# Optimization experiments

Hardware: AMD Instinct MI355X
Metric: run time of the kernel (lower is better)

The kernel has to match this reference:

```python
import jax, jax.numpy as jnp
import numpy as np

BATCH = 1024
DIM = 1024      # input_size == hidden_size (required by h0 = z.repeat(...))
BAR = 32
EPS = 1e-5


def setup_inputs() -> dict:
    key = jax.random.key(0)
    ks = jax.random.split(key, 13)
    s_in = 1.0 / np.sqrt(DIM)
    return {
        "z": jax.random.normal(ks[0], (BATCH, DIM), dtype=jnp.float32),
        "bn_gamma": jnp.ones((DIM,), jnp.float32),
        "bn_beta": jnp.zeros((DIM,), jnp.float32),
        # PyTorch LSTM params, gate order (i, f, g, o), shape (4H, in)
        "W_ih0": jax.random.uniform(ks[1], (4 * DIM, DIM), jnp.float32, -s_in, s_in),
        "W_hh0": jax.random.uniform(ks[2], (4 * DIM, DIM), jnp.float32, -s_in, s_in),
        "b_ih0": jax.random.uniform(ks[3], (4 * DIM,), jnp.float32, -s_in, s_in),
        "b_hh0": jax.random.uniform(ks[4], (4 * DIM,), jnp.float32, -s_in, s_in),
        "W_ih1": jax.random.uniform(ks[5], (4 * DIM, DIM), jnp.float32, -s_in, s_in),
        "W_hh1": jax.random.uniform(ks[6], (4 * DIM, DIM), jnp.float32, -s_in, s_in),
        "b_ih1": jax.random.uniform(ks[7], (4 * DIM,), jnp.float32, -s_in, s_in),
        "b_hh1": jax.random.uniform(ks[8], (4 * DIM,), jnp.float32, -s_in, s_in),
        "W_lin": jax.random.uniform(ks[9], (DIM, DIM), jnp.float32, -s_in, s_in),
        "b_lin": jax.random.uniform(ks[10], (DIM,), jnp.float32, -s_in, s_in),
    }


def _lstm_cell(x_proj, h, c, W_hh, b_hh):
    # x_proj already contains x @ W_ih^T + b_ih
    gates = x_proj + h @ W_hh.T + b_hh          # (B, 4H)
    i, f, g, o = jnp.split(gates, 4, axis=-1)   # PyTorch gate order i,f,g,o
    c_new = jax.nn.sigmoid(f) * c + jax.nn.sigmoid(i) * jnp.tanh(g)
    h_new = jax.nn.sigmoid(o) * jnp.tanh(c_new)
    return h_new, c_new


def reference(z, bn_gamma, bn_beta, W_ih0, W_hh0, b_ih0, b_hh0,
              W_ih1, W_hh1, b_ih1, b_hh1, W_lin, b_lin):
    # BatchNorm1d in training mode (batch statistics, biased variance)
    mean = jnp.mean(z, axis=0)
    var = jnp.var(z, axis=0)
    zn = (z - mean) * jax.lax.rsqrt(var + EPS) * bn_gamma + bn_beta  # (B, D)

    # h0 = c0 = zn for both layers (init_hidden repeats z num_hidden times)
    # Layer-0 input is the constant zn every step -> precompute its projection
    x0_proj = zn @ W_ih0.T + b_ih0  # (B, 4H)

    def step(carry, _):
        h0, c0, h1, c1 = carry
        h0, c0 = _lstm_cell(x0_proj, h0, c0, W_hh0, b_hh0)
        x1_proj = h0 @ W_ih1.T + b_ih1
        h1, c1 = _lstm_cell(x1_proj, h1, c1, W_hh1, b_hh1)
        return (h0, c0, h1, c1), h1

    _, feats = jax.lax.scan(step, (zn, zn, zn, zn), None, length=BAR)
    feat = jnp.transpose(feats, (1, 0, 2))      # (B, bar, H)
    return feat @ W_lin.T + b_lin
```

## Files before the change

kernel.cpp:

```cpp
#include <hip/hip_runtime.h>

#define DEV __device__ __forceinline__

typedef unsigned short u16;
using bf16x8 = __attribute__((ext_vector_type(8))) __bf16;
using f32x4  = __attribute__((ext_vector_type(4))) float;

DEV u16 f2bf(float f){
  unsigned u = __float_as_uint(f);
  u += 0x7fffu + ((u >> 16) & 1u);
  return (u16)(u >> 16);
}
DEV float sigf(float x){ return 1.f / (1.f + __expf(-x)); }
DEV float tanh_(float x){ return 2.f / (1.f + __expf(-2.f*x)) - 1.f; }

DEV void async16(const u16* g, u16* l){
  __builtin_amdgcn_global_load_lds(
      (const __attribute__((address_space(1))) unsigned int*)g,
      (__attribute__((address_space(3))) unsigned int*)l, 16, 0, 0);
}

__global__ void bn_stats(const float* __restrict__ z, float* __restrict__ ps, float* __restrict__ pq){
  int bx = blockIdx.x; int rg = bx >> 2, cg = bx & 3;
  int c = cg*256 + threadIdx.x;
  float s = 0.f, q = 0.f;
  for (int r = rg*64; r < rg*64 + 64; ++r){ float v = z[r*1024 + c]; s += v; q += v*v; }
  ps[rg*1024 + c] = s; pq[rg*1024 + c] = q;
}

__global__ void bn_fin(const float* __restrict__ ps, const float* __restrict__ pq,
                       const float* __restrict__ gam, const float* __restrict__ bet,
                       float* __restrict__ sc, float* __restrict__ sh){
  int c = blockIdx.x*256 + threadIdx.x;
  float s = 0.f, q = 0.f;
  for (int rg = 0; rg < 16; ++rg){ s += ps[rg*1024 + c]; q += pq[rg*1024 + c]; }
  float mean = s * (1.f/1024.f);
  float var  = q * (1.f/1024.f) - mean*mean;
  float k = gam[c] * rsqrtf(var + 1e-5f);
  sc[c] = k; sh[c] = bet[c] - mean*k;
}

__global__ void bn_norm(const float* __restrict__ z, const float* __restrict__ sc, const float* __restrict__ sh,
                        u16* __restrict__ h0, u16* __restrict__ h1,
                        float* __restrict__ c0, float* __restrict__ c1){
  int bx = blockIdx.x; int rg = bx >> 2, cg = bx & 3;
  int c = cg*256 + threadIdx.x;
  float k = sc[c], b = sh[c];
  for (int r = rg*64; r < rg*64 + 64; ++r){
    float v = z[r*1024 + c]*k + b;
    u16 hv = f2bf(v);
    h0[r*1024 + c] = hv; h1[r*1024 + c] = hv;
    c0[r*1024 + c] = v;  c1[r*1024 + c] = v;
  }
}

__global__ void conv_w(const float* __restrict__ src, u16* __restrict__ dst,
                       int dstStride, int colOff, int permute){
  int c = blockIdx.x;
  int row = c;
  if (permute){ int gate = (c>>4)&3; int u = (c&15) | ((c>>6)<<4); row = (gate<<10) + u; }
  float4 v = ((const float4*)(src + (size_t)row*1024))[threadIdx.x];
  ushort4 o; o.x = f2bf(v.x); o.y = f2bf(v.y); o.z = f2bf(v.z); o.w = f2bf(v.w);
  ((ushort4*)(dst + (size_t)c*dstStride + colOff))[threadIdx.x] = o;
}

__global__ void bias_k(const float* __restrict__ bi0, const float* __restrict__ bh0,
                       const float* __restrict__ bi1, const float* __restrict__ bh1,
                       float* __restrict__ bx0, float* __restrict__ b1){
  int c = blockIdx.x*256 + threadIdx.x;
  int gate = (c>>4)&3; int u = (c&15) | ((c>>6)<<4); int r = (gate<<10) + u;
  bx0[c] = bi0[r] + bh0[r];
  b1[c]  = bi1[r] + bh1[r];
}

template<int MODE>
DEV void gemm_core(int bx, int by,
                   const u16* __restrict__ A0, const u16* __restrict__ A1, int KloA,
                   const u16* __restrict__ Bm, int K,
                   const float* __restrict__ add, float* __restrict__ cst,
                   u16* __restrict__ hout, u16* __restrict__ hout2,
                   float* __restrict__ outf,
                   u16* sA, u16* sB)
{
  const int t = threadIdx.x;
  const int lane = t & 63;
  const int w = t >> 6, wm = w >> 1, wn = w & 1;
  const int m0 = by*128, n0 = bx*128;

  f32x4 acc[4][4];
#pragma unroll
  for (int i = 0; i < 4; ++i)
#pragma unroll
    for (int j = 0; j < 4; ++j) acc[i][j] = (f32x4){0.f,0.f,0.f,0.f};

  const int rA = t >> 2;
  const int kswz = (((t & 3) ^ ((t >> 3) & 3)) << 3);
  const int nkt = K >> 5;

  auto stage = [&](int kt, int b){
    const int k0 = kt << 5;
    const u16* aPart; int kk;
    if (k0 < KloA){ aPart = A0; kk = k0; } else { aPart = A1; kk = k0 - KloA; }
    u16* dA = sA + b*4096; u16* dB = sB + b*4096;
#pragma unroll
    for (int q = 0; q < 2; ++q){
      int row = rA + q*64;
      async16(aPart + (size_t)(m0 + row)*1024 + kk + kswz, dA + (t + q*256)*8);
      async16(Bm    + (size_t)(n0 + row)*K    + k0 + kswz, dB + (t + q*256)*8);
    }
  };

  const int rdswz = (((lane >> 4) ^ ((lane >> 1) & 3)) << 3);

  stage(0, 0);
  stage(1, 1);
  for (int kt = 0; kt < nkt; ++kt){
    if (kt + 2 < nkt){
      stage(kt + 2, (kt + 2) & 3);
      asm volatile("s_waitcnt vmcnt(8)" ::: "memory");
    } else if (kt + 1 < nkt){
      asm volatile("s_waitcnt vmcnt(4)" ::: "memory");
    } else {
      asm volatile("s_waitcnt vmcnt(0)" ::: "memory");
    }
    __builtin_amdgcn_sched_barrier(0);
    __builtin_amdgcn_s_barrier();
    __builtin_amdgcn_sched_barrier(0);

    const u16* pA = sA + (kt & 3)*4096;
    const u16* pB = sB + (kt & 3)*4096;
    bf16x8 af[4], bfr[4];
#pragma unroll
    for (int i = 0; i < 4; ++i){
      int ra = wm*64 + i*16 + (lane & 15);
      int rb = wn*64 + i*16 + (lane & 15);
      af[i]  = *(const bf16x8*)&pA[ra*32 + rdswz];
      bfr[i] = *(const bf16x8*)&pB[rb*32 + rdswz];
    }
    __builtin_amdgcn_s_setprio(1);
#pragma unroll
    for (int i = 0; i < 4; ++i)
#pragma unroll
      for (int j = 0; j < 4; ++j)
        acc[i][j] = __builtin_amdgcn_mfma_f32_16x16x32_bf16(af[i], bfr[j], acc[i][j], 0, 0, 0);
    __builtin_amdgcn_s_setprio(0);
  }

  const int s  = lane & 15;
  const int rq = (lane >> 4) * 4;

  if constexpr (MODE == 0 || MODE == 3){
    const int ldc = (MODE == 0) ? 4096 : 1024;
#pragma unroll
    for (int j = 0; j < 4; ++j){
      int col = n0 + wn*64 + j*16 + s;
      float bj = add[col];
#pragma unroll
      for (int i = 0; i < 4; ++i){
        int rowb = m0 + wm*64 + i*16 + rq;
#pragma unroll
        for (int r = 0; r < 4; ++r)
          outf[(size_t)(rowb + r)*ldc + col] = acc[i][j][r] + bj;
      }
    }
  } else {
    const int u = s + ((bx*2 + wn) << 4);
    int cidx[4]; float bj[4];
#pragma unroll
    for (int j = 0; j < 4; ++j){
      cidx[j] = n0 + wn*64 + j*16 + s;
      if (MODE == 2) bj[j] = add[cidx[j]];
    }
#pragma unroll
    for (int i = 0; i < 4; ++i){
      int rowb = m0 + wm*64 + i*16 + rq;
#pragma unroll
      for (int r = 0; r < 4; ++r){
        int row = rowb + r;
        float g0, g1, g2, g3;
        if (MODE == 1){
          const float* xp = add + (size_t)row*4096;
          g0 = acc[i][0][r] + xp[cidx[0]];
          g1 = acc[i][1][r] + xp[cidx[1]];
          g2 = acc[i][2][r] + xp[cidx[2]];
          g3 = acc[i][3][r] + xp[cidx[3]];
        } else {
          g0 = acc[i][0][r] + bj[0];
          g1 = acc[i][1][r] + bj[1];
          g2 = acc[i][2][r] + bj[2];
          g3 = acc[i][3][r] + bj[3];
        }
        float ig = sigf(g0), fg = sigf(g1), gg = tanh_(g2), og = sigf(g3);
        size_t si = (size_t)row*1024 + u;
        float cn = fg * cst[si] + ig * gg;
        cst[si] = cn;
        float hn = og * tanh_(cn);
        u16 hb = f2bf(hn);
        hout[si] = hb;
        if (MODE == 2) hout2[(size_t)row*32768 + u] = hb;
      }
    }
  }
}

template<int MODE, int SWZ>
__global__ __launch_bounds__(256)
void gemm_k(const u16* __restrict__ A0, const u16* __restrict__ Bm, int K,
            const float* __restrict__ add, float* __restrict__ outf)
{
  __shared__ __align__(16) u16 sA[4*4096];
  __shared__ __align__(16) u16 sB[4*4096];
  int bx = blockIdx.x, by = blockIdx.y;
  if constexpr (SWZ){
    int lin = by * (int)gridDim.x + bx;
    int xcd = lin & 7, idx = lin >> 3;
    by = xcd*32 + (idx >> 3);
    bx = idx & 7;
  }
  gemm_core<MODE>(bx, by, A0, nullptr, 1<<20, Bm, K, add,
                  nullptr, nullptr, nullptr, outf, sA, sB);
}

__global__ __launch_bounds__(256)
void fused_step(const u16* __restrict__ h0in, const u16* __restrict__ h1in,
                const u16* __restrict__ Whh0p, const u16* __restrict__ W1p,
                const float* __restrict__ X0p, const float* __restrict__ B1,
                float* __restrict__ C0, float* __restrict__ C1,
                u16* __restrict__ h0out, u16* __restrict__ h1out,
                u16* __restrict__ feats, int roles)
{
  __shared__ __align__(16) u16 sA[4*4096];
  __shared__ __align__(16) u16 sB[4*4096];
  int by = blockIdx.y, isL0;
  if (roles == 0){ isL0 = (by >= 8); by &= 7; }
  else isL0 = (roles == 1);
  if (isL0)
    gemm_core<1>(blockIdx.x, by, h0in, nullptr, 1<<20, Whh0p, 1024, X0p,
                 C0, h0out, nullptr, nullptr, sA, sB);
  else
    gemm_core<2>(blockIdx.x, by, h0in, h1in, 1024, W1p, 2048, B1,
                 C1, h1out, feats, nullptr, sA, sB);
}

extern "C" void kernel_launch(void* const* d_in, const int* in_sizes, int n_in,
                              void* d_out, int out_size, void* d_ws, size_t ws_size,
                              hipStream_t stream)
{
  (void)in_sizes; (void)n_in; (void)out_size; (void)ws_size;
  const float* z    = (const float*)d_in[0];
  const float* gam  = (const float*)d_in[1];
  const float* bet  = (const float*)d_in[2];
  const float* Wih0 = (const float*)d_in[3];
  const float* Whh0 = (const float*)d_in[4];
  const float* bih0 = (const float*)d_in[5];
  const float* bhh0 = (const float*)d_in[6];
  const float* Wih1 = (const float*)d_in[7];
  const float* Whh1 = (const float*)d_in[8];
  const float* bih1 = (const float*)d_in[9];
  const float* bhh1 = (const float*)d_in[10];
  const float* Wlin = (const float*)d_in[11];
  const float* blin = (const float*)d_in[12];
  float* out = (float*)d_out;

  char* p = (char*)d_ws;
  auto alloc = [&](size_t b) -> void* { void* r = (void*)p; p += (b + 255) & ~(size_t)255; return r; };
  u16*  Wih0p = (u16*)alloc((size_t)4096*1024*2);
  u16*  Whh0p = (u16*)alloc((size_t)4096*1024*2);
  u16*  W1p   = (u16*)alloc((size_t)4096*2048*2);
  u16*  Wlinp = (u16*)alloc((size_t)1024*1024*2);
  float* Bx0  = (float*)alloc(4096*4);
  float* B1   = (float*)alloc(4096*4);
  float* X0p  = (float*)alloc((size_t)1024*4096*4);
  u16*  H0a   = (u16*)alloc((size_t)1024*1024*2);
  u16*  H0b   = (u16*)alloc((size_t)1024*1024*2);
  u16*  H1a   = (u16*)alloc((size_t)1024*1024*2);
  u16*  H1b   = (u16*)alloc((size_t)1024*1024*2);
  float* C0   = (float*)alloc((size_t)1024*1024*4);
  float* C1   = (float*)alloc((size_t)1024*1024*4);
  u16*  Feats = (u16*)alloc((size_t)1024*32*1024*2);
  float* PS   = (float*)alloc(16*1024*4);
  float* PQ   = (float*)alloc(16*1024*4);
  float* Sc   = (float*)alloc(1024*4);
  float* Sh   = (float*)alloc(1024*4);

  bn_stats<<<64, 256, 0, stream>>>(z, PS, PQ);
  bn_fin<<<4, 256, 0, stream>>>(PS, PQ, gam, bet, Sc, Sh);
  bn_norm<<<64, 256, 0, stream>>>(z, Sc, Sh, H0a, H1a, C0, C1);
  conv_w<<<4096, 256, 0, stream>>>(Wih0, Wih0p, 1024, 0, 1);
  conv_w<<<4096, 256, 0, stream>>>(Whh0, Whh0p, 1024, 0, 1);
  conv_w<<<4096, 256, 0, stream>>>(Wih1, W1p, 2048, 0, 1);
  conv_w<<<4096, 256, 0, stream>>>(Whh1, W1p, 2048, 1024, 1);
  conv_w<<<1024, 256, 0, stream>>>(Wlin, Wlinp, 1024, 0, 0);
  bias_k<<<16, 256, 0, stream>>>(bih0, bhh0, bih1, bhh1, Bx0, B1);

  gemm_k<0,0><<<dim3(32,8), 256, 0, stream>>>(H0a, Wih0p, 1024, Bx0, X0p);

  u16* h0b[2] = {H0a, H0b};
  u16* h1b[2] = {H1a, H1b};

  fused_step<<<dim3(32,8), 256, 0, stream>>>(h0b[0], nullptr, Whh0p, W1p, X0p, B1,
                                             C0, C1, h0b[1], nullptr, nullptr, 1);
  for (int t = 0; t < 31; ++t){
    fused_step<<<dim3(32,16), 256, 0, stream>>>(
        h0b[(t+1)&1], h1b[t&1], Whh0p, W1p, X0p, B1,
        C0, C1, h0b[t&1], h1b[(t+1)&1], Feats + (size_t)t*1024, 0);
  }
  fused_step<<<dim3(32,8), 256, 0, stream>>>(h0b[0], h1b[1], Whh0p, W1p, X0p, B1,
                                             C0, C1, nullptr, h1b[0], Feats + (size_t)31*1024, 2);

  gemm_k<3,1><<<dim3(8,256), 256, 0, stream>>>(Feats, Wlinp, 1024, blin, out);
}
```

Baseline: 1.797 ms.

## Load GEMM A operand directly from global into registers, bypassing LDS

The A tile is no longer staged through shared memory. Each wave now loads its MFMA A fragments straight from global memory into registers, double-buffered across a main loop unrolled by two. Only the B tile still goes through LDS, which halves LDS footprint and traffic and drops the A-side LDS reads. In exchange, the two waves that share a row block each fetch the same A data from global, the fixed vmcnt waits rely on exact load counts, and the prefetch runs past the last k-tile, reading slightly out of range.

```diff
diff --git a/kernel.cpp b/kernel.cpp
--- a/kernel.cpp
+++ b/kernel.cpp
@@ -80,7 +80,7 @@
                    const float* __restrict__ add, float* __restrict__ cst,
                    u16* __restrict__ hout, u16* __restrict__ hout2,
                    float* __restrict__ outf,
-                   u16* sA, u16* sB)
+                   u16* sB)
 {
   const int t = threadIdx.x;
   const int lane = t & 63;
@@ -97,53 +97,73 @@
   const int kswz = (((t & 3) ^ ((t >> 3) & 3)) << 3);
   const int nkt = K >> 5;
 
-  auto stage = [&](int kt, int b){
+  auto stageB = [&](int kt, int b){
     const int k0 = kt << 5;
-    const u16* aPart; int kk;
-    if (k0 < KloA){ aPart = A0; kk = k0; } else { aPart = A1; kk = k0 - KloA; }
-    u16* dA = sA + b*4096; u16* dB = sB + b*4096;
-#pragma unroll
-    for (int q = 0; q < 2; ++q){
-      int row = rA + q*64;
-      async16(aPart + (size_t)(m0 + row)*1024 + kk + kswz, dA + (t + q*256)*8);
-      async16(Bm    + (size_t)(n0 + row)*K    + k0 + kswz, dB + (t + q*256)*8);
-    }
+    u16* d = sB + b*4096;
+#pragma unroll
+    for (int q = 0; q < 2; ++q)
+      async16(Bm + (size_t)(n0 + rA + q*64)*K + k0 + kswz, d + (t + q*256)*8);
   };
 
+  const int arow  = wm*64 + (lane & 15);
+  const int akoff = (lane >> 4) * 8;
+  const u16* pA0 = A0 + (size_t)(m0 + arow)*1024 + akoff;
+  const u16* pA1 = ((MODE == 2) ? A1 : A0) + (size_t)(m0 + arow)*1024 + akoff;
+
+  auto loadA = [&](bf16x8* af, int kt){
+    const int k0 = kt << 5;
+    const u16* p = (k0 < KloA) ? (pA0 + k0) : (pA1 + (k0 - KloA));
+#pragma unroll
+    for (int i = 0; i < 4; ++i) af[i] = *(const bf16x8*)(p + (size_t)i*16*1024);
+  };
+
   const int rdswz = (((lane >> 4) ^ ((lane >> 1) & 3)) << 3);
 
-  stage(0, 0);
-  stage(1, 1);
-  for (int kt = 0; kt < nkt; ++kt){
-    if (kt + 2 < nkt){
-      stage(kt + 2, (kt + 2) & 3);
-      asm volatile("s_waitcnt vmcnt(8)" ::: "memory");
-    } else if (kt + 1 < nkt){
-      asm volatile("s_waitcnt vmcnt(4)" ::: "memory");
-    } else {
-      asm volatile("s_waitcnt vmcnt(0)" ::: "memory");
-    }
+  bf16x8 afA[4], afB[4];
+  stageB(0, 0); stageB(1, 1);
+  loadA(afA, 0);
+
+  for (int kt = 0; kt < nkt; kt += 2){
+    stageB(kt + 2, (kt + 2) & 3);
+    loadA(afB, kt + 1);
+    asm volatile("s_waitcnt vmcnt(6)" ::: "memory");
     __builtin_amdgcn_sched_barrier(0);
     __builtin_amdgcn_s_barrier();
     __builtin_amdgcn_sched_barrier(0);
-
-    const u16* pA = sA + (kt & 3)*4096;
-    const u16* pB = sB + (kt & 3)*4096;
-    bf16x8 af[4], bfr[4];
-#pragma unroll
-    for (int i = 0; i < 4; ++i){
-      int ra = wm*64 + i*16 + (lane & 15);
-      int rb = wn*64 + i*16 + (lane & 15);
-      af[i]  = *(const bf16x8*)&pA[ra*32 + rdswz];
-      bfr[i] = *(const bf16x8*)&pB[rb*32 + rdswz];
-    }
-    __builtin_amdgcn_s_setprio(1);
-#pragma unroll
-    for (int i = 0; i < 4; ++i)
-#pragma unroll
-      for (int j = 0; j < 4; ++j)
-        acc[i][j] = __builtin_amdgcn_mfma_f32_16x16x32_bf16(af[i], bfr[j], acc[i][j], 0, 0, 0);
-    __builtin_amdgcn_s_setprio(0);
+    {
+      const u16* pB = sB + (kt & 3)*4096;
+      bf16x8 bfr[4];
+#pragma unroll
+      for (int i = 0; i < 4; ++i)
+        bfr[i] = *(const bf16x8*)&pB[(wn*64 + i*16 + (lane & 15))*32 + rdswz];
+      __builtin_amdgcn_s_setprio(1);
+#pragma unroll
+      for (int i = 0; i < 4; ++i)
+#pragma unroll
+        for (int j = 0; j < 4; ++j)
+          acc[i][j] = __builtin_amdgcn_mfma_f32_16x16x32_bf16(afA[i], bfr[j], acc[i][j], 0, 0, 0);
+      __builtin_amdgcn_s_setprio(0);
+    }
+    stageB(kt + 3, (kt + 3) & 3);
+    loadA(afA, kt + 2);
+    asm volatile("s_waitcnt vmcnt(6)" ::: "memory");
+    __builtin_amdgcn_sched_barrier(0);
+    __builtin_amdgcn_s_barrier();
+    __builtin_amdgcn_sched_barrier(0);
+    {
+      const u16* pB = sB + ((kt + 1) & 3)*4096;
+      bf16x8 bfr[4];
+#pragma unroll
+      for (int i = 0; i < 4; ++i)
+        bfr[i] = *(const bf16x8*)&pB[(wn*64 + i*16 + (lane & 15))*32 + rdswz];
+      __builtin_amdgcn_s_setprio(1);
+#pragma unroll
+      for (int i = 0; i < 4; ++i)
+#pragma unroll
+        for (int j = 0; j < 4; ++j)
+          acc[i][j] = __builtin_amdgcn_mfma_f32_16x16x32_bf16(afB[i], bfr[j], acc[i][j], 0, 0, 0);
+      __builtin_amdgcn_s_setprio(0);
+    }
   }
 
   const int s  = lane & 15;
@@ -208,7 +228,6 @@
 void gemm_k(const u16* __restrict__ A0, const u16* __restrict__ Bm, int K,
             const float* __restrict__ add, float* __restrict__ outf)
 {
-  __shared__ __align__(16) u16 sA[4*4096];
   __shared__ __align__(16) u16 sB[4*4096];
   int bx = blockIdx.x, by = blockIdx.y;
   if constexpr (SWZ){
@@ -218,7 +237,7 @@
     bx = idx & 7;
   }
   gemm_core<MODE>(bx, by, A0, nullptr, 1<<20, Bm, K, add,
-                  nullptr, nullptr, nullptr, outf, sA, sB);
+                  nullptr, nullptr, nullptr, outf, sB);
 }
 
 __global__ __launch_bounds__(256)
@@ -229,17 +248,16 @@
                 u16* __restrict__ h0out, u16* __restrict__ h1out,
                 u16* __restrict__ feats, int roles)
 {
-  __shared__ __align__(16) u16 sA[4*4096];
   __shared__ __align__(16) u16 sB[4*4096];
   int by = blockIdx.y, isL0;
   if (roles == 0){ isL0 = (by >= 8); by &= 7; }
   else isL0 = (roles == 1);
   if (isL0)
     gemm_core<1>(blockIdx.x, by, h0in, nullptr, 1<<20, Whh0p, 1024, X0p,
-                 C0, h0out, nullptr, nullptr, sA, sB);
+                 C0, h0out, nullptr, nullptr, sB);
   else
     gemm_core<2>(blockIdx.x, by, h0in, h1in, 1024, W1p, 2048, B1,
-                 C1, h1out, feats, nullptr, sA, sB);
+                 C1, h1out, feats, nullptr, sB);
 }
 
 extern "C" void kernel_launch(void* const* d_in, const int* in_sizes, int n_in,
```

New measurement: 2.395 ms. 33.3% more time.

## Switch GEMM core to BK=64 double-buffered pipeline with 8-way swizzle

Applied to the files above, without the earlier changes.

Replaces the 4-slot, K-step-32 prefetch-depth-2 LDS pipeline with a 2-slot, K-step-64 double buffer. The next tile is issued before computing the current one, followed by a full wait and barrier. Each barrier now covers two MFMA sub-steps, which halves the number of barriers per GEMM, and the LDS XOR swizzle is widened to 8 chunks to match the 64-wide rows. The cost is shallower latency hiding: each iteration waits for all outstanding loads before continuing.

```diff
diff --git a/kernel.cpp b/kernel.cpp
--- a/kernel.cpp
+++ b/kernel.cpp
@@ -93,57 +93,62 @@
 #pragma unroll
     for (int j = 0; j < 4; ++j) acc[i][j] = (f32x4){0.f,0.f,0.f,0.f};
 
-  const int rA = t >> 2;
-  const int kswz = (((t & 3) ^ ((t >> 3) & 3)) << 3);
-  const int nkt = K >> 5;
-
+  const int srow = t >> 3;
+  const int kswz = (((t & 7) ^ ((t >> 3) & 7)) << 3);
+  const int nkt = K >> 6;
+
+  auto stageM = [&](const u16* P, int ld, int r0, int k0, u16* dst){
+#pragma unroll
+    for (int p = 0; p < 4; ++p)
+      async16(P + (size_t)(r0 + p*32 + srow)*ld + k0 + kswz,
+              dst + p*2048 + t*8);
+  };
   auto stage = [&](int kt, int b){
-    const int k0 = kt << 5;
+    const int k0 = kt << 6;
     const u16* aPart; int kk;
     if (k0 < KloA){ aPart = A0; kk = k0; } else { aPart = A1; kk = k0 - KloA; }
-    u16* dA = sA + b*4096; u16* dB = sB + b*4096;
-#pragma unroll
-    for (int q = 0; q < 2; ++q){
-      int row = rA + q*64;
-      async16(aPart + (size_t)(m0 + row)*1024 + kk + kswz, dA + (t + q*256)*8);
-      async16(Bm    + (size_t)(n0 + row)*K    + k0 + kswz, dB + (t + q*256)*8);
-    }
+    stageM(aPart, 1024, m0, kk, sA + b*8192);
+    stageM(Bm,    K,    n0, k0, sB + b*8192);
   };
 
-  const int rdswz = (((lane >> 4) ^ ((lane >> 1) & 3)) << 3);
+  const int rsel = lane >> 4;
+  const int rxor = lane & 7;
 
   stage(0, 0);
-  stage(1, 1);
+  asm volatile("s_waitcnt vmcnt(0)" ::: "memory");
+  __builtin_amdgcn_sched_barrier(0);
+  __builtin_amdgcn_s_barrier();
+  __builtin_amdgcn_sched_barrier(0);
+
   for (int kt = 0; kt < nkt; ++kt){
-    if (kt + 2 < nkt){
-      stage(kt + 2, (kt + 2) & 3);
-      asm volatile("s_waitcnt vmcnt(8)" ::: "memory");
-    } else if (kt + 1 < nkt){
-      asm volatile("s_waitcnt vmcnt(4)" ::: "memory");
-    } else {
+    if (kt + 1 < nkt) stage(kt + 1, (kt + 1) & 1);
+    const u16* pA = sA + (kt & 1)*8192;
+    const u16* pB = sB + (kt & 1)*8192;
+#pragma unroll
+    for (int ksub = 0; ksub < 2; ++ksub){
+      bf16x8 af[4], bfr[4];
+#pragma unroll
+      for (int i = 0; i < 4; ++i){
+        int ra = wm*64 + i*16 + (lane & 15);
+        int rb = wn*64 + i*16 + (lane & 15);
+        int sl = ((ksub*4 + rsel) ^ rxor) << 3;
+        af[i]  = *(const bf16x8*)&pA[ra*64 + sl];
+        bfr[i] = *(const bf16x8*)&pB[rb*64 + sl];
+      }
+      __builtin_amdgcn_s_setprio(1);
+#pragma unroll
+      for (int i = 0; i < 4; ++i)
+#pragma unroll
+        for (int j = 0; j < 4; ++j)
+          acc[i][j] = __builtin_amdgcn_mfma_f32_16x16x32_bf16(af[i], bfr[j], acc[i][j], 0, 0, 0);
+      __builtin_amdgcn_s_setprio(0);
+    }
+    if (kt + 1 < nkt){
       asm volatile("s_waitcnt vmcnt(0)" ::: "memory");
-    }
-    __builtin_amdgcn_sched_barrier(0);
-    __builtin_amdgcn_s_barrier();
-    __builtin_amdgcn_sched_barrier(0);
-
-    const u16* pA = sA + (kt & 3)*4096;
-    const u16* pB = sB + (kt & 3)*4096;
-    bf16x8 af[4], bfr[4];
-#pragma unroll
-    for (int i = 0; i < 4; ++i){
-      int ra = wm*64 + i*16 + (lane & 15);
-      int rb = wn*64 + i*16 + (lane & 15);
-      af[i]  = *(const bf16x8*)&pA[ra*32 + rdswz];
-      bfr[i] = *(const bf16x8*)&pB[rb*32 + rdswz];
-    }
-    __builtin_amdgcn_s_setprio(1);
-#pragma unroll
-    for (int i = 0; i < 4; ++i)
-#pragma unroll
-      for (int j = 0; j < 4; ++j)
-        acc[i][j] = __builtin_amdgcn_mfma_f32_16x16x32_bf16(af[i], bfr[j], acc[i][j], 0, 0, 0);
-    __builtin_amdgcn_s_setprio(0);
+      __builtin_amdgcn_sched_barrier(0);
+      __builtin_amdgcn_s_barrier();
+      __builtin_amdgcn_sched_barrier(0);
+    }
   }
 
   const int s  = lane & 15;
@@ -208,8 +213,8 @@
 void gemm_k(const u16* __restrict__ A0, const u16* __restrict__ Bm, int K,
             const float* __restrict__ add, float* __restrict__ outf)
 {
-  __shared__ __align__(16) u16 sA[4*4096];
-  __shared__ __align__(16) u16 sB[4*4096];
+  __shared__ __align__(16) u16 sA[2*8192];
+  __shared__ __align__(16) u16 sB[2*8192];
   int bx = blockIdx.x, by = blockIdx.y;
   if constexpr (SWZ){
     int lin = by * (int)gridDim.x + bx;
@@ -229,8 +234,8 @@
                 u16* __restrict__ h0out, u16* __restrict__ h1out,
                 u16* __restrict__ feats, int roles)
 {
-  __shared__ __align__(16) u16 sA[4*4096];
-  __shared__ __align__(16) u16 sB[4*4096];
+  __shared__ __align__(16) u16 sA[2*8192];
+  __shared__ __align__(16) u16 sB[2*8192];
   int by = blockIdx.y, isL0;
   if (roles == 0){ isL0 = (by >= 8); by &= 7; }
   else isL0 = (roles == 1);
```

Result: faster. 1.745 ms (-2.9%).
